# Optimization experiments

Hardware: AMD Instinct MI355X
Metric: run time of the kernel (lower is better)

The kernel has to match this reference:

```python
import jax, jax.numpy as jnp
import numpy as np

N, D, EDIM, E, K = 10000, 64, 16, 320000, 16


def _lin(key, o, i):
    # kaiming-normal-ish init, std = sqrt(2/fan_in)
    return jax.random.normal(key, (o, i), dtype=jnp.float32) * (2.0 / i) ** 0.5


def setup_inputs() -> dict:
    key = jax.random.key(0)
    ks = jax.random.split(key, 20)
    inp = {
        "x": jax.random.normal(ks[0], (N, D), dtype=jnp.float32),
        "edge_index": jax.random.randint(ks[1], (2, E), 0, N),
        "edge_attr": jax.random.normal(ks[2], (E, EDIM), dtype=jnp.float32),
        "location_info": jax.random.uniform(ks[3], (N, 4), dtype=jnp.float32),
        "k": K,
    }
    i = 4
    for name in ["sg1", "sg2", "sg3"]:
        inp[name + "_wm"] = _lin(ks[i], D, EDIM + D); i += 1
        inp[name + "_bm"] = jnp.zeros((D,), jnp.float32)
        inp[name + "_wu"] = _lin(ks[i], D, D); i += 1
        inp[name + "_bu"] = jnp.zeros((D,), jnp.float32)
    for name in ["dg1", "dg2"]:
        inp[name + "_w1"] = _lin(ks[i], 2 * D, 2 * D); i += 1
        inp[name + "_b1"] = jnp.zeros((2 * D,), jnp.float32)
        inp[name + "_w2"] = _lin(ks[i], D, 2 * D); i += 1
        inp[name + "_b2"] = jnp.zeros((D,), jnp.float32)
    inp["f1_w"] = _lin(ks[i], D, 5 * D); i += 1
    inp["f1_b"] = jnp.zeros((D,), jnp.float32)
    inp["f2_w"] = _lin(ks[i], D, 6 * D); i += 1
    inp["f2_b"] = jnp.zeros((D,), jnp.float32)
    return inp


def _knn_edges(loc, k, n):
    # dynamic kNN on location_info (euclidean, directed src->dst, with self loops)
    loc = jax.lax.stop_gradient(loc)
    d2 = jnp.sum((loc[:, None, :] - loc[None, :, :]) ** 2, axis=-1)  # [N, N]
    d2 = jnp.where(jnp.eye(n, dtype=bool), jnp.inf, d2)
    _, idx = jax.lax.top_k(-d2, k)               # idx[i] = k nearest sources of target i
    dst = jnp.repeat(jnp.arange(n), k)
    src = idx.reshape(-1)
    loops = jnp.arange(n)
    return jnp.concatenate([src, loops]), jnp.concatenate([dst, loops])


def _forward(x, edge_index, edge_attr, location_info, k,
             sg1_wm, sg1_bm, sg1_wu, sg1_bu,
             sg2_wm, sg2_bm, sg2_wu, sg2_bu,
             sg3_wm, sg3_bm, sg3_wu, sg3_bu,
             dg1_w1, dg1_b1, dg1_w2, dg1_b2,
             dg2_w1, dg2_b1, dg2_w2, dg2_b2,
             f1_w, f1_b, f2_w, f2_b):
    n = x.shape[0]
    relu = jax.nn.relu
    s_src, s_dst = edge_index[0], edge_index[1]  # PyG: row=source j, col=target i

    def static_conv(h, wm, bm, wu, bu):
        m = relu(jnp.concatenate([edge_attr, h[s_src] - h[s_dst]], axis=1) @ wm.T + bm)
        agg = jax.ops.segment_max(m, s_dst, num_segments=n)
        agg = jnp.where(jnp.isfinite(agg), agg, 0.0)  # empty segments -> 0
        return relu(agg @ wu.T + bu)

    d_src, d_dst = _knn_edges(location_info, k, n)

    def dyn_conv(h, w1, b1, w2, b2):
        xi = h[d_dst]
        xj = h[d_src]
        m = relu(relu(jnp.concatenate([xi, xj - xi], axis=1) @ w1.T + b1) @ w2.T + b2)
        return jax.ops.segment_max(m, d_dst, num_segments=n)  # self loops => no empty segments

    h1 = static_conv(x, sg1_wm, sg1_bm, sg1_wu, sg1_bu)
    h2 = static_conv(h1, sg2_wm, sg2_bm, sg2_wu, sg2_bu)
    h3 = static_conv(h2, sg3_wm, sg3_bm, sg3_wu, sg3_bu)
    g1 = dyn_conv(h1, dg1_w1, dg1_b1, dg1_w2, dg1_b2)
    g2 = dyn_conv(g1, dg2_w1, dg2_b1, dg2_w2, dg2_b2)

    cat1 = jnp.concatenate([h1, g1, g2, h2, h3], axis=1)        # [N, 5D]
    fuse1 = relu(cat1 @ f1_w.T + f1_b)                          # [N, D]
    cat2 = jnp.concatenate([fuse1, cat1], axis=1)               # [N, 6D]
    return cat2 @ f2_w.T + f2_b                                 # [N, D]


def reference(x, edge_index, edge_attr, location_info, k,
              sg1_wm, sg1_bm, sg1_wu, sg1_bu,
              sg2_wm, sg2_bm, sg2_wu, sg2_bu,
              sg3_wm, sg3_bm, sg3_wu, sg3_bu,
              dg1_w1, dg1_b1, dg1_w2, dg1_b2,
              dg2_w1, dg2_b1, dg2_w2, dg2_b2,
              f1_w, f1_b, f2_w, f2_b):
    return _forward(x, edge_index, edge_attr, location_info, k,
                    sg1_wm, sg1_bm, sg1_wu, sg1_bu,
                    sg2_wm, sg2_bm, sg2_wu, sg2_bu,
                    sg3_wm, sg3_bm, sg3_wu, sg3_bu,
                    dg1_w1, dg1_b1, dg1_w2, dg1_b2,
                    dg2_w1, dg2_b1, dg2_w2, dg2_b2,
                    f1_w, f1_b, f2_w, f2_b)
```

## Files before the change

### kernel.cpp

```cpp
#include <hip/hip_runtime.h>

#define INF_F __builtin_inff()

typedef __attribute__((ext_vector_type(8))) short short8v;
typedef __attribute__((ext_vector_type(4))) float f32x4;
typedef unsigned long long ull;

__device__ __forceinline__ short f2bf(float x) {
  const unsigned u = __float_as_uint(x);
  return (short)((u + 0x7FFFu + ((u >> 16) & 1u)) >> 16);
}

__device__ __forceinline__ unsigned mbcnt64(ull m) {
  return __builtin_amdgcn_mbcnt_hi((unsigned)(m >> 32),
                                   __builtin_amdgcn_mbcnt_lo((unsigned)m, 0u));
}

#define KNN_G 5
#define KNN_NC (KNN_G*KNN_G*KNN_G*KNN_G)
#define KNN_PCAP 1600

__global__ __launch_bounds__(256) void count2_kernel(
    const float* __restrict__ loc, int* __restrict__ cellcount,
    int* __restrict__ cellid, int n,
    const int* __restrict__ dst, int* __restrict__ deg, int E)
{
  const int i = blockIdx.x * 256 + threadIdx.x;
  if (i < n) {
    const float4 l = *(const float4*)(loc + (size_t)i*4);
    const int cx = min(KNN_G-1, (int)(l.x * (float)KNN_G));
    const int cy = min(KNN_G-1, (int)(l.y * (float)KNN_G));
    const int cz = min(KNN_G-1, (int)(l.z * (float)KNN_G));
    const int cw = min(KNN_G-1, (int)(l.w * (float)KNN_G));
    const int c = ((cx*KNN_G + cy)*KNN_G + cz)*KNN_G + cw;
    cellid[i] = c;
    atomicAdd(&cellcount[c], 1);
  }
  if (i < E) atomicAdd(&deg[dst[i]], 1);
}

__device__ __forceinline__ void scan1b_body(
    const int* __restrict__ in, int* __restrict__ out, int n, int per)
{
  __shared__ int part[1024];
  const int t = threadIdx.x;
  const int lo = t * per, hi = min(lo + per, n);
  int sum = 0;
  for (int idx = lo; idx < hi; ++idx) sum += in[idx];
  int v = sum;
  part[t] = v;
  __syncthreads();
  for (int off = 1; off < 1024; off <<= 1) {
    const int o = (t >= off) ? part[t - off] : 0;
    __syncthreads();
    v += o;
    part[t] = v;
    __syncthreads();
  }
  int run = v - sum;
  for (int idx = lo; idx < hi; ++idx) { out[idx] = run; run += in[idx]; }
  if (t == 1023) out[n] = v;
}

__global__ __launch_bounds__(1024) void scan2_kernel(
    const int* __restrict__ inA, int* __restrict__ outA, int nA, int perA,
    const int* __restrict__ inB, int* __restrict__ outB, int nB, int perB)
{
  if (blockIdx.x == 0) scan1b_body(inA, outA, nA, perA);
  else                 scan1b_body(inB, outB, nB, perB);
}

__global__ __launch_bounds__(256) void scatter2_kernel(
    const float* __restrict__ loc, const int* __restrict__ cellid,
    const int* __restrict__ cellstart, int* __restrict__ cellfill,
    float* __restrict__ locs4s, int* __restrict__ oidx, int n,
    const int* __restrict__ srcs, const int* __restrict__ dsts,
    const int* __restrict__ rowptr, int* __restrict__ dfill,
    int* __restrict__ cs_src, int* __restrict__ cs_eid, int E)
{
  const int i = blockIdx.x * 256 + threadIdx.x;
  if (i < n) {
    const int c = cellid[i];
    const int pos = cellstart[c] + atomicAdd(&cellfill[c], 1);
    *(float4*)(locs4s + (size_t)pos*4) = *(const float4*)(loc + (size_t)i*4);
    oidx[pos] = i;
  }
  if (i < E) {
    const int d = dsts[i];
    const int pos = rowptr[d] + atomicAdd(&dfill[d], 1);
    cs_src[pos] = srcs[i];
    cs_eid[pos] = i;
  }
}

__device__ __forceinline__ ull
knn_refine16(ull* __restrict__ B, int cnt, int lane, ull& topsave)
{
  ull v[5];
#pragma unroll
  for (int s = 0; s < 5; ++s) {
    const int idx = lane + 64*s;
    v[s] = (idx < cnt) ? B[idx] : ~0ull;
  }
  ull tau = ~0ull;
#pragma unroll
  for (int r = 0; r < 16; ++r) {
    ull m = v[0]; int sl = 0;
#pragma unroll
    for (int s = 1; s < 5; ++s) if (v[s] < m) { m = v[s]; sl = s; }
    ull mm = m;
#pragma unroll
    for (int off = 32; off >= 1; off >>= 1) {
      const ull o = __shfl_xor(mm, off, 64);
      if (o < mm) mm = o;
    }
    const bool killer = (m == mm);
#pragma unroll
    for (int s = 0; s < 5; ++s) if (killer && sl == s) v[s] = ~0ull;
    if (lane == r) topsave = mm;
    tau = mm;
  }
  if (lane < 16) B[lane] = topsave;
  return tau;
}

__device__ __forceinline__ int
knn_filter(ull* __restrict__ B, int cnt, int lane, ull& tau)
{
  ull v[5];
#pragma unroll
  for (int s = 0; s < 5; ++s) {
    const int idx = lane + 64*s;
    v[s] = (idx < cnt) ? B[idx] : ~0ull;
  }
  ull g = v[0];
#pragma unroll
  for (int s = 1; s < 5; ++s) if (v[s] < g) g = v[s];
  { ull o = __shfl_xor(g, 1, 64); if (o < g) g = o;
    o = __shfl_xor(g, 2, 64); if (o < g) g = o; }
  ull t = g;
#pragma unroll
  for (int off = 4; off <= 32; off <<= 1) {
    const ull o = __shfl_xor(t, off, 64);
    if (o > t) t = o;
  }
  int nc = 0;
#pragma unroll
  for (int s = 0; s < 5; ++s) {
    const bool keep = (v[s] <= t) && (v[s] != ~0ull);
    const ull mask = __ballot(keep);
    if (mask) {
      const unsigned pre = mbcnt64(mask);
      if (keep) B[nc + pre] = v[s];
      nc += (int)__popcll(mask);
    }
  }
  tau = t;
  return nc;
}

__device__ void knn_body(int blk, ull* __restrict__ Bs, int* __restrict__ PosAll,
                         const float* __restrict__ locs4s,
                         const int* __restrict__ oidx,
                         const int* __restrict__ cellstart,
                         int* __restrict__ knn, int n)
{
#pragma clang fp contract(off)
  constexpr int TRIG = 256;
  const int wave = threadIdx.x >> 6, lane = threadIdx.x & 63;
  const int t = blk * 4 + wave;
  if (t >= n) return;
  ull* B = Bs + wave * 320;
  int* Pos = PosAll + wave * KNN_PCAP;

  const float4 L = *(const float4*)(locs4s + (size_t)t*4);
  const float tx = L.x, ty = L.y, tz = L.z, tw = L.w;
  const int cx = min(KNN_G-1, (int)(tx * (float)KNN_G));
  const int cy = min(KNN_G-1, (int)(ty * (float)KNN_G));
  const int cz = min(KNN_G-1, (int)(tz * (float)KNN_G));
  const int cw = min(KNN_G-1, (int)(tw * (float)KNN_G));

  ull tau = ~0ull;
  ull topsave = ~0ull;
  int cnt = 0;

  auto boundB = [&](int mr) -> float {
    const float w = 1.0f / (float)KNN_G;
    float Bv = INF_F;
    if (cx - mr >= 1)         Bv = fminf(Bv, tx - (float)(cx - mr) * w);
    if (cx + mr <= KNN_G - 2) Bv = fminf(Bv, (float)(cx + mr + 1) * w - tx);
    if (cy - mr >= 1)         Bv = fminf(Bv, ty - (float)(cy - mr) * w);
    if (cy + mr <= KNN_G - 2) Bv = fminf(Bv, (float)(cy + mr + 1) * w - ty);
    if (cz - mr >= 1)         Bv = fminf(Bv, tz - (float)(cz - mr) * w);
    if (cz + mr <= KNN_G - 2) Bv = fminf(Bv, (float)(cz + mr + 1) * w - tz);
    if (cw - mr >= 1)         Bv = fminf(Bv, tw - (float)(cw - mr) * w);
    if (cw + mr <= KNN_G - 2) Bv = fminf(Bv, (float)(cw + mr + 1) * w - tw);
    return Bv;
  };

  auto do_range = [&](int ps, int pe) {
    for (int p0 = ps; p0 < pe; p0 += 64) {
      const int p = p0 + lane;
      ull key = ~0ull;
      if (p < pe && p != t) {
        const float4 q = *(const float4*)(locs4s + (size_t)p*4);
        const int oj = oidx[p];
        const float a0 = q.x - tx, a1 = q.y - ty, a2 = q.z - tz, a3 = q.w - tw;
        const float s0 = a0*a0, s1 = a1*a1, s2 = a2*a2, s3 = a3*a3;
        const float d = ((s0 + s1) + s2) + s3;
        key = ((ull)__float_as_uint(d) << 32) | (unsigned)oj;
      }
      const bool surv = key < tau;
      const ull mask = __ballot(surv);
      if (mask) {
        const unsigned pre = mbcnt64(mask);
        if (surv) B[cnt + pre] = key;
        cnt += (int)__popcll(mask);
        if (cnt > TRIG) cnt = knn_filter(B, cnt, lane, tau);
      }
    }
  };

  int psv = 0, pev = 0;
  if (lane < 27) {
    const int cr = (lane == 0) ? 13 : (lane <= 13 ? lane - 1 : lane);
    const int ax = cx + (cr / 9) - 1;
    const int ay = cy + ((cr / 3) % 3) - 1;
    const int az = cz + (cr % 3) - 1;
    if (ax >= 0 && ax < KNN_G && ay >= 0 && ay < KNN_G &&
        az >= 0 && az < KNN_G) {
      const int base = ((ax*KNN_G + ay)*KNN_G + az)*KNN_G;
      const int wlo = max(cw-1, 0), whi = min(cw+1, KNN_G-1);
      psv = cellstart[base + wlo];
      pev = cellstart[base + whi + 1];
    }
  }
  const int len = max(pev - psv, 0);
  int cum = len;
#pragma unroll
  for (int off = 1; off < 64; off <<= 1) {
    const int o = __shfl_up(cum, off, 64);
    if (lane >= off) cum += o;
  }
  const int T = __shfl(cum, 63, 64);
  const int startv = cum - len;

  for (int p = psv, f = startv; p < pev && f < KNN_PCAP; ++p, ++f) Pos[f] = p;

  const int Tb = min(T, KNN_PCAP);
  const int Tm1b = Tb - 1;
  float4 qn; int ojn = 0, pgn = 0; bool vn = false;
  {
    vn = lane < Tb;
    pgn = Pos[min(lane, Tm1b)];
    qn = *(const float4*)(locs4s + (size_t)pgn*4);
    ojn = oidx[pgn];
  }
  for (int f0 = 0; f0 < Tb; f0 += 64) {
    const float4 qc = qn; const int ojc = ojn, pgc = pgn; const bool vc = vn;
    const int fN = f0 + 64 + lane;
    vn = fN < Tb;
    if (f0 + 64 < Tb) {
      pgn = Pos[min(fN, Tm1b)];
      qn = *(const float4*)(locs4s + (size_t)pgn*4);
      ojn = oidx[pgn];
    }
    ull key = ~0ull;
    if (vc && pgc != t) {
      const float a0 = qc.x - tx, a1 = qc.y - ty, a2 = qc.z - tz, a3 = qc.w - tw;
      const float s0 = a0*a0, s1 = a1*a1, s2 = a2*a2, s3 = a3*a3;
      const float d = ((s0 + s1) + s2) + s3;
      key = ((ull)__float_as_uint(d) << 32) | (unsigned)ojc;
    }
    const bool surv = key < tau;
    const ull mask = __ballot(surv);
    if (mask) {
      const unsigned pre = mbcnt64(mask);
      if (surv) B[cnt + pre] = key;
      cnt += (int)__popcll(mask);
      if (cnt > TRIG) cnt = knn_filter(B, cnt, lane, tau);
    }
  }
  if (T > KNN_PCAP) {
    for (int r = 0; r < 27; ++r) {
      const int st = __shfl(startv, r, 64);
      const int ps = __shfl(psv, r, 64);
      const int pe = __shfl(pev, r, 64);
      const int done = min(max(KNN_PCAP - st, 0), pe - ps);
      if (ps + done < pe) do_range(ps + done, pe);
    }
  }

  for (int m = 2; m <= KNN_G - 1; ++m) {
    if (cnt > 16) { tau = knn_refine16(B, cnt, lane, topsave); cnt = 16; }
    if (tau != ~0ull) {
      const float taud = __uint_as_float((unsigned)(tau >> 32));
      const float Bv = boundB(m - 1);
      if (Bv == INF_F || taud < Bv * Bv * 0.99999f) break;
    }
    const int xlo = max(cx-m, 0), xhi = min(cx+m, KNN_G-1);
    for (int ax = xlo; ax <= xhi; ++ax) {
      const bool xe = (ax == cx-m) || (ax == cx+m);
      const int ylo = max(cy-m, 0), yhi = min(cy+m, KNN_G-1);
      for (int ay = ylo; ay <= yhi; ++ay) {
        const bool ye = (ay == cy-m) || (ay == cy+m);
        const int zlo = max(cz-m, 0), zhi = min(cz+m, KNN_G-1);
        for (int az = zlo; az <= zhi; ++az) {
          const bool ze = (az == cz-m) || (az == cz+m);
          const int base = ((ax*KNN_G + ay)*KNN_G + az)*KNN_G;
          if (xe | ye | ze) {
            const int wlo = max(cw-m, 0), whi = min(cw+m, KNN_G-1);
            do_range(cellstart[base+wlo], cellstart[base+whi+1]);
          } else {
            if (cw-m >= 0) {
              const int c = base + cw - m;
              do_range(cellstart[c], cellstart[c+1]);
            }
            if (cw+m <= KNN_G-1) {
              const int c = base + cw + m;
              do_range(cellstart[c], cellstart[c+1]);
            }
          }
        }
      }
    }
  }
  (void)knn_refine16(B, cnt, lane, topsave);
  const int i = oidx[t];
  if (lane < 16) knn[(size_t)i*16 + lane] = (int)(topsave & 0xFFFFFFFFull);
}

__global__ __launch_bounds__(256) void mega_kernel(
    const float* __restrict__ locs4s, const int* __restrict__ oidx,
    const int* __restrict__ cellstart, int* __restrict__ knn, int n,
    const float* __restrict__ ea, const int* __restrict__ cs_eid,
    float* __restrict__ eac, int E,
    const float* __restrict__ w1A, const float* __restrict__ b1A,
    float* __restrict__ wpqA, float* __restrict__ bpqA,
    const float* __restrict__ w1B, const float* __restrict__ b1B,
    float* __restrict__ wpqB, float* __restrict__ bpqB,
    int KB, int EB)
{
  __shared__ ull Bs[4 * 320];
  __shared__ int Pos[4 * KNN_PCAP];
  const int bid = blockIdx.x;
  if (bid < KB) {
    knn_body(bid, Bs, Pos, locs4s, oidx, cellstart, knn, n);
  } else if (bid < KB + EB) {
    const int idx = (bid - KB) * 256 + threadIdx.x;
    if (idx < E * 4) {
      const int p = idx >> 2, c = idx & 3;
      *(float4*)(eac + (size_t)p*16 + c*4) =
          *(const float4*)(ea + (size_t)cs_eid[p]*16 + c*4);
    }
  } else {
    const int gidx = (bid - KB - EB) * 256 + threadIdx.x;
    const int l = gidx >> 13;
    const int idx = gidx & 8191;
    const float* w1 = l ? w1B : w1A;
    const float* b1 = l ? b1B : b1A;
    float* wpq = l ? wpqB : wpqA;
    float* bpq = l ? bpqB : bpqA;
    const int o = idx >> 6, i = idx & 63;
    const float a = w1[o*128 + i], b = w1[o*128 + 64 + i];
    wpq[idx] = a - b;
    wpq[128*64 + idx] = b;
    if (idx < 128) { bpq[idx] = b1[idx]; bpq[128 + idx] = 0.f; }
  }
}

__global__ __launch_bounds__(256) void static_msg_kernel(
    const float* __restrict__ R, const float* __restrict__ eac,
    const float* __restrict__ wm, const float* __restrict__ bm,
    const int* __restrict__ cs_src, const int* __restrict__ rowptr,
    float* __restrict__ agg, int n)
{
  const int wave = threadIdx.x >> 6, lane = threadIdx.x & 63;
  const int d = blockIdx.x * 4 + wave;
  if (d >= n) return;
  const int beg = rowptr[d], end = rowptr[d+1];
  const int deg = end - beg;
  const int grp = lane >> 4, li = lane & 15;

  short8v bfr[4];
#pragma unroll
  for (int nt = 0; nt < 4; ++nt) {
    short8v b = (short8v)0;
    if (grp < 2) {
      const int ch = nt*16 + li;
#pragma unroll
      for (int j = 0; j < 8; ++j) b[j] = f2bf(wm[ch*80 + grp*8 + j]);
    }
    bfr[nt] = b;
  }
  float basev[4];
#pragma unroll
  for (int nt = 0; nt < 4; ++nt) {
    const int ch = nt*16 + li;
    basev[nt] = bm[ch] - R[(size_t)d*64 + ch];
  }

  float vmax[4] = {0.f, 0.f, 0.f, 0.f};
  const f32x4 zero = (f32x4)0.f;
  for (int m0 = 0; m0 < deg; m0 += 16) {
    short8v a = (short8v)0;
    const int erow = m0 + li;
    if (grp < 2 && erow < deg) {
      const float4* ep = (const float4*)(eac + (size_t)(beg + erow)*16 + grp*8);
      const float4 q0 = ep[0], q1 = ep[1];
      a[0]=f2bf(q0.x); a[1]=f2bf(q0.y); a[2]=f2bf(q0.z); a[3]=f2bf(q0.w);
      a[4]=f2bf(q1.x); a[5]=f2bf(q1.y); a[6]=f2bf(q1.z); a[7]=f2bf(q1.w);
    }
    f32x4 Dv[4];
#pragma unroll
    for (int nt = 0; nt < 4; ++nt)
      Dv[nt] = __builtin_amdgcn_mfma_f32_16x16x32_bf16(a, bfr[nt], zero, 0, 0, 0);
#pragma unroll
    for (int j = 0; j < 4; ++j) {
      const int m = m0 + grp*4 + j;
      if (m < deg) {
        const int s = cs_src[beg + m];
        const float* Rs = R + (size_t)s*64;
#pragma unroll
        for (int nt = 0; nt < 4; ++nt) {
          const float acc = Dv[nt][j] + Rs[nt*16 + li] + basev[nt];
          vmax[nt] = fmaxf(vmax[nt], fmaxf(acc, 0.f));
        }
      }
    }
  }
#pragma unroll
  for (int nt = 0; nt < 4; ++nt) {
    float m = vmax[nt];
    m = fmaxf(m, __shfl_xor(m, 16, 64));
    m = fmaxf(m, __shfl_xor(m, 32, 64));
    vmax[nt] = m;
  }
  float r = vmax[0];
  r = (grp == 1) ? vmax[1] : r;
  r = (grp == 2) ? vmax[2] : r;
  r = (grp == 3) ? vmax[3] : r;
  agg[(size_t)d*64 + lane] = r;
}

__device__ __forceinline__ void stage_tile_bf16(
    short* __restrict__ S, const float* __restrict__ src, int srow, int sc16,
    bool valid)
{
  short tmp[16];
  if (valid) {
#pragma unroll
    for (int u = 0; u < 4; ++u) {
      const float4 v = *(const float4*)(src + u*4);
      tmp[u*4+0] = f2bf(v.x); tmp[u*4+1] = f2bf(v.y);
      tmp[u*4+2] = f2bf(v.z); tmp[u*4+3] = f2bf(v.w);
    }
  } else {
#pragma unroll
    for (int u = 0; u < 16; ++u) tmp[u] = 0;
  }
  *(short8v*)&S[srow*72 + sc16]     = *(short8v*)&tmp[0];
  *(short8v*)&S[srow*72 + sc16 + 8] = *(short8v*)&tmp[8];
}

template<bool RELU, bool ACC>
__global__ __launch_bounds__(256) void linear_kernel(
    const float* __restrict__ A, int lda,
    const float* __restrict__ W, int ldw,
    const float* __restrict__ bias,
    float* __restrict__ C, int ldc, int M, int K)
{
  __shared__ short As[64 * 72];
  __shared__ short Ws[64 * 72];
  const int tid = threadIdx.x;
  const int wave = tid >> 6, lane = tid & 63;
  const int grp = lane >> 4, li = lane & 15;
  const int m0 = blockIdx.x * 64;
  const int c0 = blockIdx.y * 64;

  f32x4 acc[4];
#pragma unroll
  for (int nt = 0; nt < 4; ++nt) acc[nt] = (f32x4)0.f;

  const int srow = tid >> 2;
  const int sc16 = (tid & 3) * 16;

  for (int kt = 0; kt < K; kt += 64) {
    const int gr = m0 + srow;
    stage_tile_bf16(As, A + (size_t)gr*lda + kt + sc16, srow, sc16, gr < M);
    stage_tile_bf16(Ws, W + (size_t)(c0 + srow)*ldw + kt + sc16, srow, sc16, true);
    __syncthreads();
#pragma unroll
    for (int ks = 0; ks < 2; ++ks) {
      const short8v a = *(const short8v*)&As[(wave*16 + li)*72 + ks*32 + grp*8];
#pragma unroll
      for (int nt = 0; nt < 4; ++nt) {
        const short8v b = *(const short8v*)&Ws[(nt*16 + li)*72 + ks*32 + grp*8];
        acc[nt] = __builtin_amdgcn_mfma_f32_16x16x32_bf16(a, b, acc[nt], 0, 0, 0);
      }
    }
    __syncthreads();
  }

#pragma unroll
  for (int nt = 0; nt < 4; ++nt) {
    const int ch = c0 + nt*16 + li;
    const float b = bias ? bias[ch] : 0.f;
#pragma unroll
    for (int j = 0; j < 4; ++j) {
      const int gr = m0 + wave*16 + grp*4 + j;
      if (gr < M) {
        float v = acc[nt][j] + b;
        if (RELU) v = fmaxf(v, 0.f);
        float* cp = C + (size_t)gr*ldc + ch;
        if (ACC) v += *cp;
        *cp = v;
      }
    }
  }
}

__global__ __launch_bounds__(256) void fused_hR_kernel(
    const float* __restrict__ A,
    const float* __restrict__ Wu, const float* __restrict__ bu,
    float* __restrict__ Hout, int ldh,
    const float* __restrict__ Wm,
    float* __restrict__ Rout, int M)
{
  __shared__ short As[64 * 72];
  __shared__ short Ws[64 * 72];
  const int tid = threadIdx.x;
  const int wave = tid >> 6, lane = tid & 63;
  const int grp = lane >> 4, li = lane & 15;
  const int m0 = blockIdx.x * 64;
  const int srow = tid >> 2;
  const int sc16 = (tid & 3) * 16;

  {
    const int gr = m0 + srow;
    stage_tile_bf16(As, A + (size_t)gr*64 + sc16, srow, sc16, gr < M);
    stage_tile_bf16(Ws, Wu + (size_t)srow*64 + sc16, srow, sc16, true);
  }
  __syncthreads();
  f32x4 acc[4];
#pragma unroll
  for (int nt = 0; nt < 4; ++nt) acc[nt] = (f32x4)0.f;
#pragma unroll
  for (int ks = 0; ks < 2; ++ks) {
    const short8v a = *(const short8v*)&As[(wave*16 + li)*72 + ks*32 + grp*8];
#pragma unroll
    for (int nt = 0; nt < 4; ++nt) {
      const short8v b = *(const short8v*)&Ws[(nt*16 + li)*72 + ks*32 + grp*8];
      acc[nt] = __builtin_amdgcn_mfma_f32_16x16x32_bf16(a, b, acc[nt], 0, 0, 0);
    }
  }
  __syncthreads();

  stage_tile_bf16(Ws, Wm + (size_t)srow*80 + sc16, srow, sc16, true);
#pragma unroll
  for (int nt = 0; nt < 4; ++nt) {
    const int ch = nt*16 + li;
    const float b = bu[ch];
#pragma unroll
    for (int j = 0; j < 4; ++j) {
      const int row = wave*16 + grp*4 + j;
      const int gr = m0 + row;
      const float v = fmaxf(acc[nt][j] + b, 0.f);
      if (gr < M) Hout[(size_t)gr*ldh + ch] = v;
      As[row*72 + ch] = f2bf(v);
    }
  }
  __syncthreads();

  f32x4 acc2[4];
#pragma unroll
  for (int nt = 0; nt < 4; ++nt) acc2[nt] = (f32x4)0.f;
#pragma unroll
  for (int ks = 0; ks < 2; ++ks) {
    const short8v a = *(const short8v*)&As[(wave*16 + li)*72 + ks*32 + grp*8];
#pragma unroll
    for (int nt = 0; nt < 4; ++nt) {
      const short8v b = *(const short8v*)&Ws[(nt*16 + li)*72 + ks*32 + grp*8];
      acc2[nt] = __builtin_amdgcn_mfma_f32_16x16x32_bf16(a, b, acc2[nt], 0, 0, 0);
    }
  }
#pragma unroll
  for (int nt = 0; nt < 4; ++nt) {
    const int ch = nt*16 + li;
#pragma unroll
    for (int j = 0; j < 4; ++j) {
      const int gr = m0 + wave*16 + grp*4 + j;
      if (gr < M) Rout[(size_t)gr*64 + ch] = acc2[nt][j];
    }
  }
}

__global__ __launch_bounds__(256) void fusion_kernel(
    const float* __restrict__ CAT,
    const float* __restrict__ f1w, const float* __restrict__ f1b,
    const float* __restrict__ f2w, const float* __restrict__ f2bias,
    float* __restrict__ out, int M)
{
  __shared__ short As[64 * 72];
  __shared__ short W1s[64 * 72];
  __shared__ short W2s[64 * 72];
  const int tid = threadIdx.x;
  const int wave = tid >> 6, lane = tid & 63;
  const int grp = lane >> 4, li = lane & 15;
  const int m0 = blockIdx.x * 64;
  const int srow = tid >> 2;
  const int sc16 = (tid & 3) * 16;

  f32x4 acc1[4], acc2[4];
#pragma unroll
  for (int nt = 0; nt < 4; ++nt) { acc1[nt] = (f32x4)0.f; acc2[nt] = (f32x4)0.f; }

  for (int kt = 0; kt < 320; kt += 64) {
    const int gr = m0 + srow;
    stage_tile_bf16(As,  CAT + (size_t)gr*320 + kt + sc16, srow, sc16, gr < M);
    stage_tile_bf16(W1s, f1w + (size_t)srow*320 + kt + sc16, srow, sc16, true);
    stage_tile_bf16(W2s, f2w + (size_t)srow*384 + 64 + kt + sc16, srow, sc16, true);
    __syncthreads();
#pragma unroll
    for (int ks = 0; ks < 2; ++ks) {
      const short8v a = *(const short8v*)&As[(wave*16 + li)*72 + ks*32 + grp*8];
#pragma unroll
      for (int nt = 0; nt < 4; ++nt) {
        const short8v b1 = *(const short8v*)&W1s[(nt*16 + li)*72 + ks*32 + grp*8];
        const short8v b2 = *(const short8v*)&W2s[(nt*16 + li)*72 + ks*32 + grp*8];
        acc1[nt] = __builtin_amdgcn_mfma_f32_16x16x32_bf16(a, b1, acc1[nt], 0, 0, 0);
        acc2[nt] = __builtin_amdgcn_mfma_f32_16x16x32_bf16(a, b2, acc2[nt], 0, 0, 0);
      }
    }
    __syncthreads();
  }

  stage_tile_bf16(W1s, f2w + (size_t)srow*384 + sc16, srow, sc16, true);
#pragma unroll
  for (int nt = 0; nt < 4; ++nt) {
    const int ch = nt*16 + li;
    const float b = f1b[ch];
#pragma unroll
    for (int j = 0; j < 4; ++j) {
      const int row = wave*16 + grp*4 + j;
      const float v = fmaxf(acc1[nt][j] + b, 0.f);
      As[row*72 + ch] = f2bf(v);
    }
  }
  __syncthreads();
#pragma unroll
  for (int ks = 0; ks < 2; ++ks) {
    const short8v a = *(const short8v*)&As[(wave*16 + li)*72 + ks*32 + grp*8];
#pragma unroll
    for (int nt = 0; nt < 4; ++nt) {
      const short8v b = *(const short8v*)&W1s[(nt*16 + li)*72 + ks*32 + grp*8];
      acc2[nt] = __builtin_amdgcn_mfma_f32_16x16x32_bf16(a, b, acc2[nt], 0, 0, 0);
    }
  }
#pragma unroll
  for (int nt = 0; nt < 4; ++nt) {
    const int ch = nt*16 + li;
    const float b = f2bias[ch];
#pragma unroll
    for (int j = 0; j < 4; ++j) {
      const int gr = m0 + wave*16 + grp*4 + j;
      if (gr < M) out[(size_t)gr*64 + ch] = acc2[nt][j] + b;
    }
  }
}

#define TPW 4

__global__ __launch_bounds__(256) void dyn_mfma_kernel(
    const float* __restrict__ PQ,
    const float* __restrict__ W2, const float* __restrict__ b2,
    const int* __restrict__ knn, float* __restrict__ out, int ldo, int n)
{
  __shared__ short w2s[64 * 136];
  __shared__ short Ts[4][17 * 136];
  const int tid = threadIdx.x;
  const int wave = tid >> 6, lane = tid & 63;

  for (int idx = tid; idx < 64 * 128; idx += 256) {
    const int c = idx >> 7, k = idx & 127;
    w2s[c*136 + k] = f2bf(W2[c*128 + k]);
  }
  __syncthreads();

  short8v bfr[4][4];
#pragma unroll
  for (int nt = 0; nt < 4; ++nt)
#pragma unroll
    for (int kt = 0; kt < 4; ++kt)
      bfr[nt][kt] = *(const short8v*)&w2s[(nt*16 + (lane&15))*136 +
                                          kt*32 + (lane>>4)*8];
  const float b2v = b2[lane];
  short* T = Ts[wave];

  for (int tg = 0; tg < TPW; ++tg) {
    const int i = (blockIdx.x * 4 + wave) * TPW + tg;
    if (i >= n) break;
    const size_t i16 = (size_t)i * 16;

    for (int s = 0; s < 9; ++s) {
      const int slot = lane + 64*s;
      if (slot < 544) {
        const int row = slot >> 5, k4 = slot & 31;
        const int j = (row < 16) ? knn[i16 + row] : i;
        const float4 p = *(const float4*)(PQ + (size_t)i*256 + k4*4);
        const float4 q = *(const float4*)(PQ + (size_t)j*256 + 128 + k4*4);
        const float t0 = fmaxf(p.x + q.x, 0.f), t1 = fmaxf(p.y + q.y, 0.f);
        const float t2 = fmaxf(p.z + q.z, 0.f), t3 = fmaxf(p.w + q.w, 0.f);
        int2 w;
        w.x = ((int)(unsigned short)f2bf(t1) << 16) | (unsigned short)f2bf(t0);
        w.y = ((int)(unsigned short)f2bf(t3) << 16) | (unsigned short)f2bf(t2);
        *(int2*)&T[row*136 + k4*4] = w;
      }
    }

    f32x4 acc0[4], acc1[4];
#pragma unroll
    for (int nt = 0; nt < 4; ++nt) {
      acc0[nt] = (f32x4)0.f;
      acc1[nt] = (f32x4)0.f;
    }
#pragma unroll
    for (int kt = 0; kt < 4; ++kt) {
      const short8v a1 = *(const short8v*)&T[(lane&15)*136 + kt*32 + (lane>>4)*8];
      const short8v a2 = *(const short8v*)&T[16*136 + kt*32 + (lane>>4)*8];
#pragma unroll
      for (int nt = 0; nt < 4; ++nt) {
        acc0[nt] = __builtin_amdgcn_mfma_f32_16x16x32_bf16(a1, bfr[nt][kt], acc0[nt], 0, 0, 0);
        acc1[nt] = __builtin_amdgcn_mfma_f32_16x16x32_bf16(a2, bfr[nt][kt], acc1[nt], 0, 0, 0);
      }
    }

    float v[4];
#pragma unroll
    for (int nt = 0; nt < 4; ++nt) {
      float m = fmaxf(fmaxf(acc0[nt][0], acc0[nt][1]),
                      fmaxf(acc0[nt][2], acc0[nt][3]));
      m = fmaxf(m, acc1[nt][0]);
      m = fmaxf(m, __shfl_xor(m, 16, 64));
      m = fmaxf(m, __shfl_xor(m, 32, 64));
      v[nt] = m;
    }
    const int g = lane >> 4;
    float r = v[0];
    r = (g == 1) ? v[1] : r;
    r = (g == 2) ? v[2] : r;
    r = (g == 3) ? v[3] : r;
    out[(size_t)i*ldo + lane] = fmaxf(r + b2v, 0.f);
  }
}

extern "C" void kernel_launch(void* const* d_in, const int* in_sizes, int n_in,
                              void* d_out, int out_size, void* d_ws, size_t ws_size,
                              hipStream_t stream)
{
  const float* x   = (const float*)d_in[0];
  const int*   ei  = (const int*)d_in[1];
  const float* ea  = (const float*)d_in[2];
  const float* loc = (const float*)d_in[3];
  const float* sg_wm[3] = {(const float*)d_in[5],  (const float*)d_in[9],  (const float*)d_in[13]};
  const float* sg_bm[3] = {(const float*)d_in[6],  (const float*)d_in[10], (const float*)d_in[14]};
  const float* sg_wu[3] = {(const float*)d_in[7],  (const float*)d_in[11], (const float*)d_in[15]};
  const float* sg_bu[3] = {(const float*)d_in[8],  (const float*)d_in[12], (const float*)d_in[16]};
  const float* dg_w1[2] = {(const float*)d_in[17], (const float*)d_in[21]};
  const float* dg_b1[2] = {(const float*)d_in[18], (const float*)d_in[22]};
  const float* dg_w2[2] = {(const float*)d_in[19], (const float*)d_in[23]};
  const float* dg_b2[2] = {(const float*)d_in[20], (const float*)d_in[24]};
  const float* f1_w = (const float*)d_in[25];
  const float* f1_b = (const float*)d_in[26];
  const float* f2_w = (const float*)d_in[27];
  const float* f2_b = (const float*)d_in[28];
  float* out = (float*)d_out;

  const int n    = in_sizes[0] / 64;
  const int Etot = in_sizes[1] / 2;
  const int* srcp = ei;
  const int* dstp = ei + Etot;

  char* basep = (char*)d_ws;
  size_t cur = 0;
  auto alloc = [&](size_t bytes) -> void* {
    void* p = basep + cur;
    cur = (cur + bytes + 255) & ~(size_t)255;
    return p;
  };
  float* CAT  = (float*)alloc((size_t)n * 320 * 4);
  float* Rb   = (float*)alloc((size_t)n * 64 * 4);
  float* PQb  = (float*)alloc((size_t)n * 256 * 4);
  float* agg  = (float*)alloc((size_t)n * 64 * 4);
  float* wpq[2];
  float* bpq[2];
  wpq[0] = (float*)alloc(256 * 64 * 4);  bpq[0] = (float*)alloc(256 * 4);
  wpq[1] = (float*)alloc(256 * 64 * 4);  bpq[1] = (float*)alloc(256 * 4);
  int* knnb   = (int*)alloc((size_t)n * 16 * 4);
  int* zeros     = (int*)alloc((size_t)(2*KNN_NC + 2*n) * 4);
  int* cellcount = zeros;
  int* cellfill  = zeros + KNN_NC;
  int* deg       = zeros + 2*KNN_NC;
  int* dfill     = zeros + 2*KNN_NC + n;
  int* cellstart = (int*)alloc((size_t)(KNN_NC + 1) * 4);
  int* cellidb   = (int*)alloc((size_t)n * 4);
  float* locs4s  = (float*)alloc((size_t)n * 4 * 4);
  int* oidx      = (int*)alloc((size_t)n * 4);
  int* rowptr    = (int*)alloc((size_t)(n + 1) * 4);
  int* cs_src    = (int*)alloc((size_t)Etot * 4);
  int* cs_eid    = (int*)alloc((size_t)Etot * 4);
  float* ea_csr  = (float*)alloc((size_t)Etot * 16 * 4);
  (void)ws_size; (void)n_in; (void)out_size;

  const int nbE = (Etot + 255) / 256;

  hipMemsetAsync(zeros, 0, (size_t)(2*KNN_NC + 2*n) * 4, stream);
  count2_kernel<<<nbE, 256, 0, stream>>>(loc, cellcount, cellidb, n,
                                         dstp, deg, Etot);
  scan2_kernel<<<2, 1024, 0, stream>>>(cellcount, cellstart, KNN_NC,
                                       (KNN_NC + 1023) / 1024,
                                       deg, rowptr, n, (n + 1023) / 1024);
  scatter2_kernel<<<nbE, 256, 0, stream>>>(loc, cellidb, cellstart, cellfill,
                                           locs4s, oidx, n,
                                           srcp, dstp, rowptr, dfill,
                                           cs_src, cs_eid, Etot);
  const int KB = (n + 3) / 4;
  const int EB = (Etot * 4 + 255) / 256;
  mega_kernel<<<KB + EB + 64, 256, 0, stream>>>(
      locs4s, oidx, cellstart, knnb, n,
      ea, cs_eid, ea_csr, Etot,
      dg_w1[0], dg_b1[0], wpq[0], bpq[0],
      dg_w1[1], dg_b1[1], wpq[1], bpq[1],
      KB, EB);

  const int mb = (n + 63) / 64;
  auto lin = [&](const float* A, int lda, const float* W, int ldw, const float* bias,
                 float* C, int ldc, int K, int ncols, bool relu) {
    dim3 grid(mb, ncols / 64);
    if (relu) linear_kernel<true,  false><<<grid, 256, 0, stream>>>(A, lda, W, ldw, bias, C, ldc, n, K);
    else      linear_kernel<false, false><<<grid, 256, 0, stream>>>(A, lda, W, ldw, bias, C, ldc, n, K);
  };

  lin(x, 64, sg_wm[0] + 16, 80, nullptr, Rb, 64, 64, 64, false);
  static_msg_kernel<<<(n + 3) / 4, 256, 0, stream>>>(Rb, ea_csr, sg_wm[0],
                                                     sg_bm[0], cs_src,
                                                     rowptr, agg, n);
  fused_hR_kernel<<<mb, 256, 0, stream>>>(agg, sg_wu[0], sg_bu[0],
                                          CAT + 0, 320,
                                          sg_wm[1] + 16, Rb, n);
  static_msg_kernel<<<(n + 3) / 4, 256, 0, stream>>>(Rb, ea_csr, sg_wm[1],
                                                     sg_bm[1], cs_src,
                                                     rowptr, agg, n);
  fused_hR_kernel<<<mb, 256, 0, stream>>>(agg, sg_wu[1], sg_bu[1],
                                          CAT + 192, 320,
                                          sg_wm[2] + 16, Rb, n);
  static_msg_kernel<<<(n + 3) / 4, 256, 0, stream>>>(Rb, ea_csr, sg_wm[2],
                                                     sg_bm[2], cs_src,
                                                     rowptr, agg, n);
  lin(agg, 64, sg_wu[2], 64, sg_bu[2], CAT + 256, 320, 64, 64, true);

  const float* din[2] = {CAT + 0, CAT + 64};
  float* doutp[2] = {CAT + 64, CAT + 128};
  const int db = (n + 4*TPW - 1) / (4*TPW);
  for (int l = 0; l < 2; ++l) {
    lin(din[l], 320, wpq[l], 64, bpq[l], PQb, 256, 64, 256, false);
    dyn_mfma_kernel<<<db, 256, 0, stream>>>(PQb, dg_w2[l], dg_b2[l],
                                            knnb, doutp[l], 320, n);
  }

  fusion_kernel<<<mb, 256, 0, stream>>>(CAT, f1_w, f1_b, f2_w, f2_b, out, n);
}
```

Before: 312.8 us.

## Fold first static projection into mega kernel and h3 linear into fusion

The x→R projection for the first static conv now runs as extra blocks inside mega_kernel, which gets a shared byte buffer reused across its roles. The final static conv's update linear (agg→h3 with ReLU) now runs inside fusion_kernel through an extra LDS tile, so h3 is never written to or read back from CAT. static_msg_kernel also processes two destination nodes per wave, reusing the bf16 weight fragments it loads. Together these remove two kernel launches and one global round-trip of h3, at the cost of fewer, longer static-message waves and more LDS in the fusion kernel.

```diff
diff --git a/kernel.cpp b/kernel.cpp
--- a/kernel.cpp
+++ b/kernel.cpp
@@ -330,6 +330,26 @@
   if (lane < 16) knn[(size_t)i*16 + lane] = (int)(topsave & 0xFFFFFFFFull);
 }
 
+__device__ __forceinline__ void stage_tile_bf16(
+    short* __restrict__ S, const float* __restrict__ src, int srow, int sc16,
+    bool valid)
+{
+  short tmp[16];
+  if (valid) {
+#pragma unroll
+    for (int u = 0; u < 4; ++u) {
+      const float4 v = *(const float4*)(src + u*4);
+      tmp[u*4+0] = f2bf(v.x); tmp[u*4+1] = f2bf(v.y);
+      tmp[u*4+2] = f2bf(v.z); tmp[u*4+3] = f2bf(v.w);
+    }
+  } else {
+#pragma unroll
+    for (int u = 0; u < 16; ++u) tmp[u] = 0;
+  }
+  *(short8v*)&S[srow*72 + sc16]     = *(short8v*)&tmp[0];
+  *(short8v*)&S[srow*72 + sc16 + 8] = *(short8v*)&tmp[8];
+}
+
 __global__ __launch_bounds__(256) void mega_kernel(
     const float* __restrict__ locs4s, const int* __restrict__ oidx,
     const int* __restrict__ cellstart, int* __restrict__ knn, int n,
@@ -339,13 +359,15 @@
     float* __restrict__ wpqA, float* __restrict__ bpqA,
     const float* __restrict__ w1B, const float* __restrict__ b1B,
     float* __restrict__ wpqB, float* __restrict__ bpqB,
+    const float* __restrict__ x, const float* __restrict__ wm1,
+    float* __restrict__ Rout,
     int KB, int EB)
 {
-  __shared__ ull Bs[4 * 320];
-  __shared__ int Pos[4 * KNN_PCAP];
+  __shared__ __align__(16) char smem[4*320*8 + 4*KNN_PCAP*4];
   const int bid = blockIdx.x;
   if (bid < KB) {
-    knn_body(bid, Bs, Pos, locs4s, oidx, cellstart, knn, n);
+    knn_body(bid, (ull*)smem, (int*)(smem + 4*320*8),
+             locs4s, oidx, cellstart, knn, n);
   } else if (bid < KB + EB) {
     const int idx = (bid - KB) * 256 + threadIdx.x;
     if (idx < E * 4) {
@@ -353,7 +375,7 @@
       *(float4*)(eac + (size_t)p*16 + c*4) =
           *(const float4*)(ea + (size_t)cs_eid[p]*16 + c*4);
     }
-  } else {
+  } else if (bid < KB + EB + 64) {
     const int gidx = (bid - KB - EB) * 256 + threadIdx.x;
     const int l = gidx >> 13;
     const int idx = gidx & 8191;
@@ -366,8 +388,44 @@
     wpq[idx] = a - b;
     wpq[128*64 + idx] = b;
     if (idx < 128) { bpq[idx] = b1[idx]; bpq[128 + idx] = 0.f; }
-  }
-}
+  } else {
+    short* As = (short*)smem;
+    short* Ws = (short*)(smem + 64*72*2);
+    const int tid = threadIdx.x;
+    const int wave = tid >> 6, lane = tid & 63;
+    const int grp = lane >> 4, li = lane & 15;
+    const int m0 = (bid - KB - EB - 64) * 64;
+    const int srow = tid >> 2;
+    const int sc16 = (tid & 3) * 16;
+    const int gr = m0 + srow;
+    stage_tile_bf16(As, x + (size_t)gr*64 + sc16, srow, sc16, gr < n);
+    stage_tile_bf16(Ws, wm1 + (size_t)srow*80 + sc16, srow, sc16, true);
+    __syncthreads();
+    f32x4 acc[4];
+#pragma unroll
+    for (int nt = 0; nt < 4; ++nt) acc[nt] = (f32x4)0.f;
+#pragma unroll
+    for (int ks = 0; ks < 2; ++ks) {
+      const short8v a = *(const short8v*)&As[(wave*16 + li)*72 + ks*32 + grp*8];
+#pragma unroll
+      for (int nt = 0; nt < 4; ++nt) {
+        const short8v b = *(const short8v*)&Ws[(nt*16 + li)*72 + ks*32 + grp*8];
+        acc[nt] = __builtin_amdgcn_mfma_f32_16x16x32_bf16(a, b, acc[nt], 0, 0, 0);
+      }
+    }
+#pragma unroll
+    for (int nt = 0; nt < 4; ++nt) {
+      const int ch = nt*16 + li;
+#pragma unroll
+      for (int j = 0; j < 4; ++j) {
+        const int r = m0 + wave*16 + grp*4 + j;
+        if (r < n) Rout[(size_t)r*64 + ch] = acc[nt][j];
+      }
+    }
+  }
+}
+
+#define TPW_S 2
 
 __global__ __launch_bounds__(256) void static_msg_kernel(
     const float* __restrict__ R, const float* __restrict__ eac,
@@ -376,13 +434,10 @@
     float* __restrict__ agg, int n)
 {
   const int wave = threadIdx.x >> 6, lane = threadIdx.x & 63;
-  const int d = blockIdx.x * 4 + wave;
-  if (d >= n) return;
-  const int beg = rowptr[d], end = rowptr[d+1];
-  const int deg = end - beg;
   const int grp = lane >> 4, li = lane & 15;
 
   short8v bfr[4];
+  float bmv[4];
 #pragma unroll
   for (int nt = 0; nt < 4; ++nt) {
     short8v b = (short8v)0;
@@ -392,78 +447,64 @@
       for (int j = 0; j < 8; ++j) b[j] = f2bf(wm[ch*80 + grp*8 + j]);
     }
     bfr[nt] = b;
-  }
-  float basev[4];
-#pragma unroll
-  for (int nt = 0; nt < 4; ++nt) {
-    const int ch = nt*16 + li;
-    basev[nt] = bm[ch] - R[(size_t)d*64 + ch];
-  }
-
-  float vmax[4] = {0.f, 0.f, 0.f, 0.f};
+    bmv[nt] = bm[nt*16 + li];
+  }
   const f32x4 zero = (f32x4)0.f;
-  for (int m0 = 0; m0 < deg; m0 += 16) {
-    short8v a = (short8v)0;
-    const int erow = m0 + li;
-    if (grp < 2 && erow < deg) {
-      const float4* ep = (const float4*)(eac + (size_t)(beg + erow)*16 + grp*8);
-      const float4 q0 = ep[0], q1 = ep[1];
-      a[0]=f2bf(q0.x); a[1]=f2bf(q0.y); a[2]=f2bf(q0.z); a[3]=f2bf(q0.w);
-      a[4]=f2bf(q1.x); a[5]=f2bf(q1.y); a[6]=f2bf(q1.z); a[7]=f2bf(q1.w);
-    }
-    f32x4 Dv[4];
+
+  for (int tg = 0; tg < TPW_S; ++tg) {
+    const int d = (blockIdx.x * 4 + wave) * TPW_S + tg;
+    if (d >= n) break;
+    const int beg = rowptr[d], end = rowptr[d+1];
+    const int deg = end - beg;
+    float basev[4];
 #pragma unroll
     for (int nt = 0; nt < 4; ++nt)
-      Dv[nt] = __builtin_amdgcn_mfma_f32_16x16x32_bf16(a, bfr[nt], zero, 0, 0, 0);
-#pragma unroll
-    for (int j = 0; j < 4; ++j) {
-      const int m = m0 + grp*4 + j;
-      if (m < deg) {
-        const int s = cs_src[beg + m];
-        const float* Rs = R + (size_t)s*64;
-#pragma unroll
-        for (int nt = 0; nt < 4; ++nt) {
-          const float acc = Dv[nt][j] + Rs[nt*16 + li] + basev[nt];
-          vmax[nt] = fmaxf(vmax[nt], fmaxf(acc, 0.f));
+      basev[nt] = bmv[nt] - R[(size_t)d*64 + nt*16 + li];
+
+    float vmax[4] = {0.f, 0.f, 0.f, 0.f};
+    for (int m0 = 0; m0 < deg; m0 += 16) {
+      short8v a = (short8v)0;
+      const int erow = m0 + li;
+      if (grp < 2 && erow < deg) {
+        const float4* ep = (const float4*)(eac + (size_t)(beg + erow)*16 + grp*8);
+        const float4 q0 = ep[0], q1 = ep[1];
+        a[0]=f2bf(q0.x); a[1]=f2bf(q0.y); a[2]=f2bf(q0.z); a[3]=f2bf(q0.w);
+        a[4]=f2bf(q1.x); a[5]=f2bf(q1.y); a[6]=f2bf(q1.z); a[7]=f2bf(q1.w);
+      }
+      f32x4 Dv[4];
+#pragma unroll
+      for (int nt = 0; nt < 4; ++nt)
+        Dv[nt] = __builtin_amdgcn_mfma_f32_16x16x32_bf16(a, bfr[nt], zero, 0, 0, 0);
+#pragma unroll
+      for (int j = 0; j < 4; ++j) {
+        const int m = m0 + grp*4 + j;
+        if (m < deg) {
+          const int s = cs_src[beg + m];
+          const float* Rs = R + (size_t)s*64;
+#pragma unroll
+          for (int nt = 0; nt < 4; ++nt) {
+            const float acc = Dv[nt][j] + Rs[nt*16 + li] + basev[nt];
+            vmax[nt] = fmaxf(vmax[nt], fmaxf(acc, 0.f));
+          }
         }
       }
     }
-  }
-#pragma unroll
-  for (int nt = 0; nt < 4; ++nt) {
-    float m = vmax[nt];
-    m = fmaxf(m, __shfl_xor(m, 16, 64));
-    m = fmaxf(m, __shfl_xor(m, 32, 64));
-    vmax[nt] = m;
-  }
-  float r = vmax[0];
-  r = (grp == 1) ? vmax[1] : r;
-  r = (grp == 2) ? vmax[2] : r;
-  r = (grp == 3) ? vmax[3] : r;
-  agg[(size_t)d*64 + lane] = r;
-}
-
-__device__ __forceinline__ void stage_tile_bf16(
-    short* __restrict__ S, const float* __restrict__ src, int srow, int sc16,
-    bool valid)
-{
-  short tmp[16];
-  if (valid) {
-#pragma unroll
-    for (int u = 0; u < 4; ++u) {
-      const float4 v = *(const float4*)(src + u*4);
-      tmp[u*4+0] = f2bf(v.x); tmp[u*4+1] = f2bf(v.y);
-      tmp[u*4+2] = f2bf(v.z); tmp[u*4+3] = f2bf(v.w);
-    }
-  } else {
-#pragma unroll
-    for (int u = 0; u < 16; ++u) tmp[u] = 0;
-  }
-  *(short8v*)&S[srow*72 + sc16]     = *(short8v*)&tmp[0];
-  *(short8v*)&S[srow*72 + sc16 + 8] = *(short8v*)&tmp[8];
-}
-
-template<bool RELU, bool ACC>
+#pragma unroll
+    for (int nt = 0; nt < 4; ++nt) {
+      float m = vmax[nt];
+      m = fmaxf(m, __shfl_xor(m, 16, 64));
+      m = fmaxf(m, __shfl_xor(m, 32, 64));
+      vmax[nt] = m;
+    }
+    float r = vmax[0];
+    r = (grp == 1) ? vmax[1] : r;
+    r = (grp == 2) ? vmax[2] : r;
+    r = (grp == 3) ? vmax[3] : r;
+    agg[(size_t)d*64 + lane] = r;
+  }
+}
+
+template<bool RELU>
 __global__ __launch_bounds__(256) void linear_kernel(
     const float* __restrict__ A, int lda,
     const float* __restrict__ W, int ldw,
@@ -512,9 +553,7 @@
       if (gr < M) {
         float v = acc[nt][j] + b;
         if (RELU) v = fmaxf(v, 0.f);
-        float* cp = C + (size_t)gr*ldc + ch;
-        if (ACC) v += *cp;
-        *cp = v;
+        C[(size_t)gr*ldc + ch] = v;
       }
     }
   }
@@ -597,6 +636,8 @@
 
 __global__ __launch_bounds__(256) void fusion_kernel(
     const float* __restrict__ CAT,
+    const float* __restrict__ aggv,
+    const float* __restrict__ wu3, const float* __restrict__ bu3,
     const float* __restrict__ f1w, const float* __restrict__ f1b,
     const float* __restrict__ f2w, const float* __restrict__ f2bias,
     float* __restrict__ out, int M)
@@ -604,6 +645,7 @@
   __shared__ short As[64 * 72];
   __shared__ short W1s[64 * 72];
   __shared__ short W2s[64 * 72];
+  __shared__ short H3s[64 * 72];
   const int tid = threadIdx.x;
   const int wave = tid >> 6, lane = tid & 63;
   const int grp = lane >> 4, li = lane & 15;
@@ -611,19 +653,51 @@
   const int srow = tid >> 2;
   const int sc16 = (tid & 3) * 16;
 
+  {
+    const int gr = m0 + srow;
+    stage_tile_bf16(As,  aggv + (size_t)gr*64 + sc16, srow, sc16, gr < M);
+    stage_tile_bf16(W1s, wu3 + (size_t)srow*64 + sc16, srow, sc16, true);
+  }
+  __syncthreads();
   f32x4 acc1[4], acc2[4];
 #pragma unroll
   for (int nt = 0; nt < 4; ++nt) { acc1[nt] = (f32x4)0.f; acc2[nt] = (f32x4)0.f; }
-
-  for (int kt = 0; kt < 320; kt += 64) {
-    const int gr = m0 + srow;
-    stage_tile_bf16(As,  CAT + (size_t)gr*320 + kt + sc16, srow, sc16, gr < M);
+#pragma unroll
+  for (int ks = 0; ks < 2; ++ks) {
+    const short8v a = *(const short8v*)&As[(wave*16 + li)*72 + ks*32 + grp*8];
+#pragma unroll
+    for (int nt = 0; nt < 4; ++nt) {
+      const short8v b = *(const short8v*)&W1s[(nt*16 + li)*72 + ks*32 + grp*8];
+      acc1[nt] = __builtin_amdgcn_mfma_f32_16x16x32_bf16(a, b, acc1[nt], 0, 0, 0);
+    }
+  }
+#pragma unroll
+  for (int nt = 0; nt < 4; ++nt) {
+    const int ch = nt*16 + li;
+    const float b = bu3[ch];
+#pragma unroll
+    for (int j = 0; j < 4; ++j) {
+      const int row = wave*16 + grp*4 + j;
+      H3s[row*72 + ch] = f2bf(fmaxf(acc1[nt][j] + b, 0.f));
+    }
+  }
+  __syncthreads();
+
+#pragma unroll
+  for (int nt = 0; nt < 4; ++nt) acc1[nt] = (f32x4)0.f;
+  for (int tile = 0; tile < 5; ++tile) {
+    const int kt = tile * 64;
+    if (tile < 4) {
+      const int gr = m0 + srow;
+      stage_tile_bf16(As, CAT + (size_t)gr*320 + kt + sc16, srow, sc16, gr < M);
+    }
     stage_tile_bf16(W1s, f1w + (size_t)srow*320 + kt + sc16, srow, sc16, true);
     stage_tile_bf16(W2s, f2w + (size_t)srow*384 + 64 + kt + sc16, srow, sc16, true);
     __syncthreads();
+    const short* Ause = (tile < 4) ? As : H3s;
 #pragma unroll
     for (int ks = 0; ks < 2; ++ks) {
-      const short8v a = *(const short8v*)&As[(wave*16 + li)*72 + ks*32 + grp*8];
+      const short8v a = *(const short8v*)&Ause[(wave*16 + li)*72 + ks*32 + grp*8];
 #pragma unroll
       for (int nt = 0; nt < 4; ++nt) {
         const short8v b1 = *(const short8v*)&W1s[(nt*16 + li)*72 + ks*32 + grp*8];
@@ -643,8 +717,7 @@
 #pragma unroll
     for (int j = 0; j < 4; ++j) {
       const int row = wave*16 + grp*4 + j;
-      const float v = fmaxf(acc1[nt][j] + b, 0.f);
-      As[row*72 + ch] = f2bf(v);
+      As[row*72 + ch] = f2bf(fmaxf(acc1[nt][j] + b, 0.f));
     }
   }
   __syncthreads();
@@ -813,6 +886,7 @@
   (void)ws_size; (void)n_in; (void)out_size;
 
   const int nbE = (Etot + 255) / 256;
+  const int mb = (n + 63) / 64;
 
   hipMemsetAsync(zeros, 0, (size_t)(2*KNN_NC + 2*n) * 4, stream);
   count2_kernel<<<nbE, 256, 0, stream>>>(loc, cellcount, cellidb, n,
@@ -826,38 +900,34 @@
                                            cs_src, cs_eid, Etot);
   const int KB = (n + 3) / 4;
   const int EB = (Etot * 4 + 255) / 256;
-  mega_kernel<<<KB + EB + 64, 256, 0, stream>>>(
+  mega_kernel<<<KB + EB + 64 + mb, 256, 0, stream>>>(
       locs4s, oidx, cellstart, knnb, n,
       ea, cs_eid, ea_csr, Etot,
       dg_w1[0], dg_b1[0], wpq[0], bpq[0],
       dg_w1[1], dg_b1[1], wpq[1], bpq[1],
+      x, sg_wm[0] + 16, Rb,
       KB, EB);
 
-  const int mb = (n + 63) / 64;
   auto lin = [&](const float* A, int lda, const float* W, int ldw, const float* bias,
                  float* C, int ldc, int K, int ncols, bool relu) {
     dim3 grid(mb, ncols / 64);
-    if (relu) linear_kernel<true,  false><<<grid, 256, 0, stream>>>(A, lda, W, ldw, bias, C, ldc, n, K);
-    else      linear_kernel<false, false><<<grid, 256, 0, stream>>>(A, lda, W, ldw, bias, C, ldc, n, K);
+    if (relu) linear_kernel<true ><<<grid, 256, 0, stream>>>(A, lda, W, ldw, bias, C, ldc, n, K);
+    else      linear_kernel<false><<<grid, 256, 0, stream>>>(A, lda, W, ldw, bias, C, ldc, n, K);
   };
 
-  lin(x, 64, sg_wm[0] + 16, 80, nullptr, Rb, 64, 64, 64, false);
-  static_msg_kernel<<<(n + 3) / 4, 256, 0, stream>>>(Rb, ea_csr, sg_wm[0],
-                                                     sg_bm[0], cs_src,
-                                                     rowptr, agg, n);
+  const int smb = (n + 4*TPW_S - 1) / (4*TPW_S);
+  static_msg_kernel<<<smb, 256, 0, stream>>>(Rb, ea_csr, sg_wm[0], sg_bm[0],
+                                             cs_src, rowptr, agg, n);
   fused_hR_kernel<<<mb, 256, 0, stream>>>(agg, sg_wu[0], sg_bu[0],
                                           CAT + 0, 320,
                                           sg_wm[1] + 16, Rb, n);
-  static_msg_kernel<<<(n + 3) / 4, 256, 0, stream>>>(Rb, ea_csr, sg_wm[1],
-                                                     sg_bm[1], cs_src,
-                                                     rowptr, agg, n);
+  static_msg_kernel<<<smb, 256, 0, stream>>>(Rb, ea_csr, sg_wm[1], sg_bm[1],
+                                             cs_src, rowptr, agg, n);
   fused_hR_kernel<<<mb, 256, 0, stream>>>(agg, sg_wu[1], sg_bu[1],
                                           CAT + 192, 320,
                                           sg_wm[2] + 16, Rb, n);
-  static_msg_kernel<<<(n + 3) / 4, 256, 0, stream>>>(Rb, ea_csr, sg_wm[2],
-                                                     sg_bm[2], cs_src,
-                                                     rowptr, agg, n);
-  lin(agg, 64, sg_wu[2], 64, sg_bu[2], CAT + 256, 320, 64, 64, true);
+  static_msg_kernel<<<smb, 256, 0, stream>>>(Rb, ea_csr, sg_wm[2], sg_bm[2],
+                                             cs_src, rowptr, agg, n);
 
   const float* din[2] = {CAT + 0, CAT + 64};
   float* doutp[2] = {CAT + 64, CAT + 128};
@@ -868,5 +938,6 @@
                                             knnb, doutp[l], 320, n);
   }
 
-  fusion_kernel<<<mb, 256, 0, stream>>>(CAT, f1_w, f1_b, f2_w, f2_b, out, n);
-}
+  fusion_kernel<<<mb, 256, 0, stream>>>(CAT, agg, sg_wu[2], sg_bu[2],
+                                        f1_w, f1_b, f2_w, f2_b, out, n);
+}
```

Result: faster. 300.8 us (-3.9%).
